# Kernel optimization log

Measured on AMD Instinct MI355X. Metric: run time of the kernel, lower is better.

Reference implementation:

```python
import jax, jax.numpy as jnp
import numpy as np

B, T, C, H = 4, 2048, 1024, 16
HD = C // H
INIT_SCALE = 0.25

def setup_inputs() -> dict:
    key = jax.random.key(0)
    k1, k2, k3 = jax.random.split(key, 3)
    x = jax.random.normal(k1, (B, T, C), dtype=jnp.float32)
    W_attn = jax.random.normal(k2, (3 * C, C), dtype=jnp.float32) * INIT_SCALE  # torch Linear weight [out,in]
    b_attn = jnp.zeros((3 * C,), dtype=jnp.float32)
    W_proj = jax.random.normal(k3, (C, C), dtype=jnp.float32) * INIT_SCALE
    b_proj = jnp.zeros((C,), dtype=jnp.float32)
    return {"x": x, "W_attn": W_attn, "b_attn": b_attn, "W_proj": W_proj, "b_proj": b_proj}

def reference(x, W_attn, b_attn, W_proj, b_proj):
    # fused QKV projection: [B,T,3C]
    qkv = x @ W_attn.T + b_attn
    q, k, v = jnp.split(qkv, 3, axis=-1)  # each [B,T,C]
    # [B,H,T,HD]
    q = q.reshape(B, T, H, HD).transpose(0, 2, 1, 3)
    k = k.reshape(B, T, H, HD).transpose(0, 2, 1, 3)
    v = v.reshape(B, T, H, HD).transpose(0, 2, 1, 3)
    scale = 1.0 / jnp.sqrt(jnp.asarray(HD, dtype=q.dtype))
    attn = jnp.einsum('bhqd,bhkd->bhqk', q, k) * scale  # [B,H,T,T]
    attn = jax.nn.softmax(attn, axis=-1)
    out = jnp.einsum('bhqk,bhkd->bhqd', attn, v)  # [B,H,T,HD]
    out = out.transpose(0, 2, 1, 3).reshape(B, T, C)
    return out @ W_proj.T + b_proj
```

## Files before the change

### kernel.cpp

```cpp
#include <hip/hip_runtime.h>
#include <hip/hip_bf16.h>

#define BB 4
#define TT 2048
#define CC 1024
#define HH 16
#define HD 64

typedef _Float16 half8 __attribute__((ext_vector_type(8)));
typedef _Float16 half4 __attribute__((ext_vector_type(4)));
typedef _Float16 half2_t __attribute__((ext_vector_type(2)));
typedef __fp16 fp16x2 __attribute__((ext_vector_type(2)));
typedef float floatx4 __attribute__((ext_vector_type(4)));
typedef float floatx16 __attribute__((ext_vector_type(16)));
typedef int intx2 __attribute__((ext_vector_type(2)));
typedef int intx4 __attribute__((ext_vector_type(4)));

__device__ __forceinline__ void async_cp16(const void* g, void* l) {
    __builtin_amdgcn_global_load_lds(
        (const __attribute__((address_space(1))) unsigned int*)g,
        (__attribute__((address_space(3))) unsigned int*)l,
        16, 0, 0);
}

__device__ __forceinline__ float exp2_raw(float x) {
    return __builtin_amdgcn_exp2f(x);
}

__device__ __forceinline__ int pkh(float a, float b) {
    fp16x2 v = __builtin_amdgcn_cvt_pkrtz(a, b);
    return __builtin_bit_cast(int, v);
}

__device__ __forceinline__ float maxv16(floatx16 s) {
    float a0 = fmaxf(fmaxf(s[0], s[1]), s[2]);
    float a1 = fmaxf(fmaxf(s[3], s[4]), s[5]);
    float a2 = fmaxf(fmaxf(s[6], s[7]), s[8]);
    float a3 = fmaxf(fmaxf(s[9], s[10]), s[11]);
    float a4 = fmaxf(fmaxf(s[12], s[13]), s[14]);
    float b0 = fmaxf(fmaxf(a0, a1), a2);
    float b1 = fmaxf(fmaxf(a3, a4), s[15]);
    return fmaxf(b0, b1);
}

__device__ __forceinline__ half8 assembleF(int a, int b, int c, int d) {
    intx2 s1 = __builtin_amdgcn_permlane32_swap(a, c, false, false);
    intx2 s2 = __builtin_amdgcn_permlane32_swap(b, d, false, false);
    intx4 w = {s1[0], s2[0], s1[1], s2[1]};
    return __builtin_bit_cast(half8, w);
}

__global__ void cvt_f32_f16(const float* __restrict__ src, _Float16* __restrict__ dst, int n) {
    int i = (blockIdx.x * blockDim.x + threadIdx.x) * 8;
    if (i < n) {
        float4 v0 = *(const float4*)(src + i);
        float4 v1 = *(const float4*)(src + i + 4);
        half8 h;
        h[0] = (_Float16)v0.x; h[1] = (_Float16)v0.y; h[2] = (_Float16)v0.z; h[3] = (_Float16)v0.w;
        h[4] = (_Float16)v1.x; h[5] = (_Float16)v1.y; h[6] = (_Float16)v1.z; h[7] = (_Float16)v1.w;
        *(half8*)(dst + i) = h;
    }
}

template <int EPI>
__global__ __launch_bounds__(256) void hgemm_nt(
    const _Float16* __restrict__ A, const _Float16* __restrict__ Bw,
    const float* __restrict__ bias,
    _Float16* __restrict__ q_out, _Float16* __restrict__ k_out, _Float16* __restrict__ v_out,
    float* __restrict__ c_out,
    int M, int N, int K)
{
    __shared__ __attribute__((aligned(16))) _Float16 As[2 * 128 * 32];
    __shared__ __attribute__((aligned(16))) _Float16 Bs[2 * 128 * 32];

    const int tid  = threadIdx.x;
    const int lane = tid & 63;
    const int wave = tid >> 6;
    const int quad = lane >> 4;
    const int lc   = lane & 15;
    const int wr   = wave >> 1, wc = wave & 1;
    const size_t bm = (size_t)blockIdx.y * 128;
    const size_t bn = (size_t)blockIdx.x * 128;

    const int r0 = tid >> 2;
    const int ck = (tid & 3) * 8;

    const _Float16* Ap = A + (bm + r0) * (size_t)K + ck;
    const _Float16* Bp = Bw + (bn + r0) * (size_t)K + ck;
    _Float16* lA = As + tid * 8;
    _Float16* lB = Bs + tid * 8;
    const size_t rstep = (size_t)64 * K;

    floatx4 acc[4][4] = {};

    for (int kk = 0; kk < K; kk += 64) {
        __syncthreads();
        async_cp16(Ap + kk, lA);
        async_cp16(Ap + kk + rstep, lA + 2048);
        async_cp16(Ap + kk + 32, lA + 4096);
        async_cp16(Ap + kk + 32 + rstep, lA + 4096 + 2048);
        async_cp16(Bp + kk, lB);
        async_cp16(Bp + kk + rstep, lB + 2048);
        async_cp16(Bp + kk + 32, lB + 4096);
        async_cp16(Bp + kk + 32 + rstep, lB + 4096 + 2048);
        __syncthreads();

#pragma unroll
        for (int h = 0; h < 2; h++) {
            half8 af[4], bf[4];
#pragma unroll
            for (int mt = 0; mt < 4; mt++)
                af[mt] = *(const half8*)(As + h * 4096 + (wr * 64 + mt * 16 + lc) * 32 + quad * 8);
#pragma unroll
            for (int nt = 0; nt < 4; nt++)
                bf[nt] = *(const half8*)(Bs + h * 4096 + (wc * 64 + nt * 16 + lc) * 32 + quad * 8);
#pragma unroll
            for (int mt = 0; mt < 4; mt++)
#pragma unroll
                for (int nt = 0; nt < 4; nt++)
                    acc[mt][nt] = __builtin_amdgcn_mfma_f32_16x16x32_f16(af[mt], bf[nt], acc[mt][nt], 0, 0, 0);
        }
    }

#pragma unroll
    for (int mt = 0; mt < 4; mt++) {
        int mbase = (int)bm + wr * 64 + mt * 16 + quad * 4;
#pragma unroll
        for (int nt = 0; nt < 4; nt++) {
            int n = (int)bn + wc * 64 + nt * 16 + lc;
            float bv = bias[n];
#pragma unroll
            for (int r = 0; r < 4; r++) {
                float v = acc[mt][nt][r] + bv;
                int mm = mbase + r;
                if (EPI == 0) {
                    int seg = n >> 10;
                    int cm  = n & 1023;
                    int h = cm >> 6, d = cm & 63;
                    int bb = mm >> 11, t = mm & 2047;
                    size_t dst = (((size_t)(bb * HH + h)) * TT + t) * HD + d;
                    if (seg == 0)      q_out[dst] = (_Float16)(v * 0.18033688f);
                    else if (seg == 1) k_out[dst] = (_Float16)v;
                    else               v_out[dst] = (_Float16)v;
                } else {
                    c_out[(size_t)mm * N + n] = v;
                }
            }
        }
    }
}

__global__ __launch_bounds__(512) void attn_flash(
    const _Float16* __restrict__ Qp, const _Float16* __restrict__ Kp,
    const _Float16* __restrict__ Vp, _Float16* __restrict__ Op)
{
    __shared__ __attribute__((aligned(16))) _Float16 Ks[64 * 64];
    __shared__ __attribute__((aligned(16))) _Float16 Vt[64 * 64];

    const int bh   = blockIdx.x;
    const int qt   = blockIdx.y;
    const int tid  = threadIdx.x;
    const int lane = tid & 63;
    const int wave = tid >> 6;
    const int ql   = lane & 31;
    const int hi   = lane >> 5;

    const size_t hb = (size_t)bh * TT * HD;

    const int qrow = qt * 256 + wave * 32 + ql;
    half8 bq[4];
#pragma unroll
    for (int c = 0; c < 4; c++)
        bq[c] = *(const half8*)(Qp + hb + (size_t)qrow * HD + c * 16 + hi * 8);

    floatx16 o0 = (floatx16)0.0f, o1 = (floatx16)0.0f;
    float mrun = -1e30f, lrun = 0.f;

    const int sk = tid >> 3;
    const int sj = tid & 7;
    const int sg = sj ^ (sk & 7);
    const _Float16* Kg = Kp + hb + (size_t)sk * HD + sg * 8;
    _Float16* KsW = Ks + tid * 8;

    const int vkp = tid >> 4;
    const int vd4 = (tid & 15) * 4;
    const _Float16* Vg0 = Vp + hb + (size_t)(2 * vkp) * HD + vd4;
    const _Float16* Vg1 = Vg0 + HD;

    half8 kv  = *(const half8*)Kg;
    half4 va0 = *(const half4*)Vg0;
    half4 vb0 = *(const half4*)Vg1;

    for (int kt = 0; kt < TT; kt += 64) {
        __syncthreads();
        *(half8*)KsW = kv;
#pragma unroll
        for (int j = 0; j < 4; j++) {
            int row = vd4 + j;
            int boff = (row * 128 + vkp * 4) ^ (((row >> 2) & 7) << 4);
            half2_t w; w[0] = va0[j]; w[1] = vb0[j];
            *(half2_t*)((char*)Vt + boff) = w;
        }
        __syncthreads();

        if (kt + 64 < TT) {
            const size_t koff = (size_t)(kt + 64) * HD;
            kv  = *(const half8*)(Kg + koff);
            va0 = *(const half4*)(Vg0 + koff);
            vb0 = *(const half4*)(Vg1 + koff);
        }

        floatx16 s0 = (floatx16)0.0f, s1 = (floatx16)0.0f;
        __builtin_amdgcn_s_setprio(1);
#pragma unroll
        for (int c = 0; c < 4; c++) {
            int offk = (ql * 128 + c * 32 + hi * 16) ^ ((ql & 7) << 4);
            half8 a0 = *(const half8*)((const char*)Ks + offk);
            half8 a1 = *(const half8*)((const char*)Ks + offk + 4096);
            s0 = __builtin_amdgcn_mfma_f32_32x32x16_f16(a0, bq[c], s0, 0, 0, 0);
            s1 = __builtin_amdgcn_mfma_f32_32x32x16_f16(a1, bq[c], s1, 0, 0, 0);
        }
        __builtin_amdgcn_s_setprio(0);

        float mx = fmaxf(maxv16(s0), maxv16(s1));
        mx = fmaxf(mx, __shfl_xor(mx, 32));
        const bool noresc = __all(mx <= mrun + 8.0f);
        const float mnew = noresc ? mrun : fmaxf(mrun, mx);
        float rs = 0.f;
        int d[16];
#pragma unroll
        for (int i = 0; i < 8; i++) {
            float e0 = exp2_raw(s0[2 * i] - mnew);
            float e1 = exp2_raw(s0[2 * i + 1] - mnew);
            rs += e0 + e1;
            d[i] = pkh(e0, e1);
        }
#pragma unroll
        for (int i = 0; i < 8; i++) {
            float e0 = exp2_raw(s1[2 * i] - mnew);
            float e1 = exp2_raw(s1[2 * i + 1] - mnew);
            rs += e0 + e1;
            d[8 + i] = pkh(e0, e1);
        }
        rs += __shfl_xor(rs, 32);
        if (!noresc) {
            float al = exp2_raw(mrun - mnew);
            mrun = mnew;
            lrun *= al;
            o0 *= al;
            o1 *= al;
        }
        lrun += rs;

        half8 F[4];
        F[0] = assembleF(d[0], d[1], d[2], d[3]);
        F[1] = assembleF(d[4], d[5], d[6], d[7]);
        F[2] = assembleF(d[8], d[9], d[10], d[11]);
        F[3] = assembleF(d[12], d[13], d[14], d[15]);

        __builtin_amdgcn_s_setprio(1);
#pragma unroll
        for (int kb = 0; kb < 4; kb++) {
            int offv = (ql * 128 + kb * 32 + hi * 16) ^ (((ql >> 2) & 7) << 4);
            half8 v0 = *(const half8*)((const char*)Vt + offv);
            half8 v1 = *(const half8*)((const char*)Vt + offv + 4096);
            o0 = __builtin_amdgcn_mfma_f32_32x32x16_f16(v0, F[kb], o0, 0, 0, 0);
            o1 = __builtin_amdgcn_mfma_f32_32x32x16_f16(v1, F[kb], o1, 0, 0, 0);
        }
        __builtin_amdgcn_s_setprio(0);
    }

    const float inv = __builtin_amdgcn_rcpf(lrun);
    const int b = bh >> 4, h = bh & 15;
    size_t base = ((size_t)(b * TT + qrow)) * CC + h * HD;
#pragma unroll
    for (int rr = 0; rr < 4; rr++) {
        half4 hv0, hv1;
#pragma unroll
        for (int t = 0; t < 4; t++) {
            hv0[t] = (_Float16)(o0[rr * 4 + t] * inv);
            hv1[t] = (_Float16)(o1[rr * 4 + t] * inv);
        }
        *(half4*)(Op + base + 8 * rr + 4 * hi) = hv0;
        *(half4*)(Op + base + 32 + 8 * rr + 4 * hi) = hv1;
    }
}

extern "C" void kernel_launch(void* const* d_in, const int* in_sizes, int n_in,
                              void* d_out, int out_size, void* d_ws, size_t ws_size,
                              hipStream_t stream) {
    const float* x      = (const float*)d_in[0];
    const float* W_attn = (const float*)d_in[1];
    const float* b_attn = (const float*)d_in[2];
    const float* W_proj = (const float*)d_in[3];
    const float* b_proj = (const float*)d_in[4];
    float* out = (float*)d_out;

    const size_t SZ_XH  = (size_t)BB * TT * CC * 2;
    const size_t SZ_WA  = (size_t)3 * CC * CC * 2;
    const size_t SZ_WP  = (size_t)CC * CC * 2;
    const size_t SZ_QKV = (size_t)BB * HH * TT * HD * 2;
    size_t off = 0;
    _Float16* xh  = (_Float16*)((char*)d_ws + off); off += SZ_XH;
    _Float16* wah = (_Float16*)((char*)d_ws + off); off += SZ_WA;
    _Float16* wph = (_Float16*)((char*)d_ws + off); off += SZ_WP;
    _Float16* Qh  = (_Float16*)((char*)d_ws + off); off += SZ_QKV;
    _Float16* Kh  = (_Float16*)((char*)d_ws + off); off += SZ_QKV;
    _Float16* Vh  = (_Float16*)((char*)d_ws + off); off += SZ_QKV;
    _Float16* Ah  = (_Float16*)((char*)d_ws + off); off += SZ_XH;
    if (ws_size < off) return;

    const int NX  = BB * TT * CC;
    const int NWA = 3 * CC * CC;
    const int NWP = CC * CC;
    cvt_f32_f16<<<NX / 8 / 256, 256, 0, stream>>>(x, xh, NX);
    cvt_f32_f16<<<NWA / 8 / 256, 256, 0, stream>>>(W_attn, wah, NWA);
    cvt_f32_f16<<<NWP / 8 / 256, 256, 0, stream>>>(W_proj, wph, NWP);

    hgemm_nt<0><<<dim3(3 * CC / 128, BB * TT / 128), 256, 0, stream>>>(
        xh, wah, b_attn, Qh, Kh, Vh, nullptr, BB * TT, 3 * CC, CC);

    attn_flash<<<dim3(BB * HH, TT / 256), 512, 0, stream>>>(Qh, Kh, Vh, Ah);

    hgemm_nt<1><<<dim3(CC / 128, BB * TT / 128), 256, 0, stream>>>(
        Ah, wph, b_proj, nullptr, nullptr, nullptr, out, BB * TT, CC, CC);
}
```

Measured before the change: 276.2 us.

## Fuse conversion kernels, remap GEMM blocks, double-buffer attention K/V tiles

The three fp32-to-fp16 conversion launches become one kernel that picks its source buffer by index, removing two launches. The GEMM remaps its flat block index so blocks are spread in strides of eight across the grid, likely aimed at cache locality across the XCDs. The attention kernel double-buffers its K and V LDS tiles so the next tile is written while the current one is used, dropping one barrier per iteration at the cost of twice the LDS.

```diff
diff --git a/kernel.cpp b/kernel.cpp
--- a/kernel.cpp
+++ b/kernel.cpp
@@ -50,16 +50,26 @@
     return __builtin_bit_cast(half8, w);
 }
 
-__global__ void cvt_f32_f16(const float* __restrict__ src, _Float16* __restrict__ dst, int n) {
+#define NX  (BB * TT * CC)
+#define NWA (3 * CC * CC)
+#define NWP (CC * CC)
+__global__ void cvt_all(const float* __restrict__ x, const float* __restrict__ wa,
+                        const float* __restrict__ wp,
+                        _Float16* __restrict__ xh, _Float16* __restrict__ wah,
+                        _Float16* __restrict__ wph) {
     int i = (blockIdx.x * blockDim.x + threadIdx.x) * 8;
-    if (i < n) {
-        float4 v0 = *(const float4*)(src + i);
-        float4 v1 = *(const float4*)(src + i + 4);
-        half8 h;
-        h[0] = (_Float16)v0.x; h[1] = (_Float16)v0.y; h[2] = (_Float16)v0.z; h[3] = (_Float16)v0.w;
-        h[4] = (_Float16)v1.x; h[5] = (_Float16)v1.y; h[6] = (_Float16)v1.z; h[7] = (_Float16)v1.w;
-        *(half8*)(dst + i) = h;
-    }
+    const float* src;
+    _Float16* dst;
+    int j;
+    if (i < NX)            { src = x;  dst = xh;  j = i; }
+    else if (i < NX + NWA) { src = wa; dst = wah; j = i - NX; }
+    else                   { src = wp; dst = wph; j = i - NX - NWA; }
+    float4 v0 = *(const float4*)(src + j);
+    float4 v1 = *(const float4*)(src + j + 4);
+    half8 h;
+    h[0] = (_Float16)v0.x; h[1] = (_Float16)v0.y; h[2] = (_Float16)v0.z; h[3] = (_Float16)v0.w;
+    h[4] = (_Float16)v1.x; h[5] = (_Float16)v1.y; h[6] = (_Float16)v1.z; h[7] = (_Float16)v1.w;
+    *(half8*)(dst + j) = h;
 }
 
 template <int EPI>
@@ -79,8 +89,12 @@
     const int quad = lane >> 4;
     const int lc   = lane & 15;
     const int wr   = wave >> 1, wc = wave & 1;
-    const size_t bm = (size_t)blockIdx.y * 128;
-    const size_t bn = (size_t)blockIdx.x * 128;
+
+    const int nwg = gridDim.x * gridDim.y;
+    int flat = blockIdx.y * gridDim.x + blockIdx.x;
+    flat = (flat & 7) * (nwg >> 3) + (flat >> 3);
+    const size_t bm = (size_t)(flat / gridDim.x) * 128;
+    const size_t bn = (size_t)(flat % gridDim.x) * 128;
 
     const int r0 = tid >> 2;
     const int ck = (tid & 3) * 8;
@@ -154,8 +168,8 @@
     const _Float16* __restrict__ Qp, const _Float16* __restrict__ Kp,
     const _Float16* __restrict__ Vp, _Float16* __restrict__ Op)
 {
-    __shared__ __attribute__((aligned(16))) _Float16 Ks[64 * 64];
-    __shared__ __attribute__((aligned(16))) _Float16 Vt[64 * 64];
+    __shared__ __attribute__((aligned(16))) _Float16 Ks[2][64 * 64];
+    __shared__ __attribute__((aligned(16))) _Float16 Vt[2][64 * 64];
 
     const int bh   = blockIdx.x;
     const int qt   = blockIdx.y;
@@ -180,7 +194,6 @@
     const int sj = tid & 7;
     const int sg = sj ^ (sk & 7);
     const _Float16* Kg = Kp + hb + (size_t)sk * HD + sg * 8;
-    _Float16* KsW = Ks + tid * 8;
 
     const int vkp = tid >> 4;
     const int vd4 = (tid & 15) * 4;
@@ -190,33 +203,52 @@
     half8 kv  = *(const half8*)Kg;
     half4 va0 = *(const half4*)Vg0;
     half4 vb0 = *(const half4*)Vg1;
-
+    *(half8*)(Ks[0] + tid * 8) = kv;
+#pragma unroll
+    for (int j = 0; j < 4; j++) {
+        int row = vd4 + j;
+        int boff = (row * 128 + vkp * 4) ^ (((row >> 2) & 7) << 4);
+        half2_t w; w[0] = va0[j]; w[1] = vb0[j];
+        *(half2_t*)((char*)Vt[0] + boff) = w;
+    }
+    {
+        const size_t koff = (size_t)64 * HD;
+        kv  = *(const half8*)(Kg + koff);
+        va0 = *(const half4*)(Vg0 + koff);
+        vb0 = *(const half4*)(Vg1 + koff);
+    }
+
+    int cur = 0;
     for (int kt = 0; kt < TT; kt += 64) {
         __syncthreads();
-        *(half8*)KsW = kv;
-#pragma unroll
-        for (int j = 0; j < 4; j++) {
-            int row = vd4 + j;
-            int boff = (row * 128 + vkp * 4) ^ (((row >> 2) & 7) << 4);
-            half2_t w; w[0] = va0[j]; w[1] = vb0[j];
-            *(half2_t*)((char*)Vt + boff) = w;
-        }
-        __syncthreads();
 
         if (kt + 64 < TT) {
-            const size_t koff = (size_t)(kt + 64) * HD;
-            kv  = *(const half8*)(Kg + koff);
-            va0 = *(const half4*)(Vg0 + koff);
-            vb0 = *(const half4*)(Vg1 + koff);
-        }
+            *(half8*)(Ks[cur ^ 1] + tid * 8) = kv;
+#pragma unroll
+            for (int j = 0; j < 4; j++) {
+                int row = vd4 + j;
+                int boff = (row * 128 + vkp * 4) ^ (((row >> 2) & 7) << 4);
+                half2_t w; w[0] = va0[j]; w[1] = vb0[j];
+                *(half2_t*)((char*)Vt[cur ^ 1] + boff) = w;
+            }
+            if (kt + 128 < TT) {
+                const size_t koff = (size_t)(kt + 128) * HD;
+                kv  = *(const half8*)(Kg + koff);
+                va0 = *(const half4*)(Vg0 + koff);
+                vb0 = *(const half4*)(Vg1 + koff);
+            }
+        }
+
+        const char* Kbuf = (const char*)Ks[cur];
+        const char* Vbuf = (const char*)Vt[cur];
 
         floatx16 s0 = (floatx16)0.0f, s1 = (floatx16)0.0f;
         __builtin_amdgcn_s_setprio(1);
 #pragma unroll
         for (int c = 0; c < 4; c++) {
             int offk = (ql * 128 + c * 32 + hi * 16) ^ ((ql & 7) << 4);
-            half8 a0 = *(const half8*)((const char*)Ks + offk);
-            half8 a1 = *(const half8*)((const char*)Ks + offk + 4096);
+            half8 a0 = *(const half8*)(Kbuf + offk);
+            half8 a1 = *(const half8*)(Kbuf + offk + 4096);
             s0 = __builtin_amdgcn_mfma_f32_32x32x16_f16(a0, bq[c], s0, 0, 0, 0);
             s1 = __builtin_amdgcn_mfma_f32_32x32x16_f16(a1, bq[c], s1, 0, 0, 0);
         }
@@ -262,12 +294,14 @@
 #pragma unroll
         for (int kb = 0; kb < 4; kb++) {
             int offv = (ql * 128 + kb * 32 + hi * 16) ^ (((ql >> 2) & 7) << 4);
-            half8 v0 = *(const half8*)((const char*)Vt + offv);
-            half8 v1 = *(const half8*)((const char*)Vt + offv + 4096);
+            half8 v0 = *(const half8*)(Vbuf + offv);
+            half8 v1 = *(const half8*)(Vbuf + offv + 4096);
             o0 = __builtin_amdgcn_mfma_f32_32x32x16_f16(v0, F[kb], o0, 0, 0, 0);
             o1 = __builtin_amdgcn_mfma_f32_32x32x16_f16(v1, F[kb], o1, 0, 0, 0);
         }
         __builtin_amdgcn_s_setprio(0);
+
+        cur ^= 1;
     }
 
     const float inv = __builtin_amdgcn_rcpf(lrun);
@@ -310,12 +344,8 @@
     _Float16* Ah  = (_Float16*)((char*)d_ws + off); off += SZ_XH;
     if (ws_size < off) return;
 
-    const int NX  = BB * TT * CC;
-    const int NWA = 3 * CC * CC;
-    const int NWP = CC * CC;
-    cvt_f32_f16<<<NX / 8 / 256, 256, 0, stream>>>(x, xh, NX);
-    cvt_f32_f16<<<NWA / 8 / 256, 256, 0, stream>>>(W_attn, wah, NWA);
-    cvt_f32_f16<<<NWP / 8 / 256, 256, 0, stream>>>(W_proj, wph, NWP);
+    const int NTOT = NX + NWA + NWP;
+    cvt_all<<<NTOT / 8 / 256, 256, 0, stream>>>(x, W_attn, W_proj, xh, wah, wph);
 
     hgemm_nt<0><<<dim3(3 * CC / 128, BB * TT / 128), 256, 0, stream>>>(
         xh, wah, b_attn, Qh, Kh, Vh, nullptr, BB * TT, 3 * CC, CC);
```

New measurement: 271.1 us. Within noise of the previous version (-1.9%).
